# Optimization experiments

Measured on AMD Instinct MI355X. Metric: run time of the kernel, lower is better.

## Reference

```python
import jax, jax.numpy as jnp
import numpy as np

NUM_ITER = 10
NUM_LAYER = 3
EMB_DIM = 128
ALPHA = 0.1
NUM_ATOM_FEATS = 9
ATOM_VOCAB = 119
N_NODES = 50000
N_EDGES = 800000


def setup_inputs() -> dict:
    key = jax.random.key(0)
    ks = jax.random.split(key, 5)
    x = jax.random.randint(ks[0], (N_NODES, NUM_ATOM_FEATS), 0, ATOM_VOCAB, dtype=jnp.int64 if jax.config.jax_enable_x64 else jnp.int32)
    edge_index = jax.random.randint(ks[1], (2, N_EDGES), 0, N_NODES, dtype=jnp.int32)
    scale = 1.0 / np.sqrt(EMB_DIM)
    atom_emb = jax.random.normal(ks[2], (NUM_ATOM_FEATS, ATOM_VOCAB, EMB_DIM), dtype=jnp.float32) * 0.1
    Ws = jax.random.normal(ks[3], (NUM_LAYER, EMB_DIM, EMB_DIM), dtype=jnp.float32) * scale
    bs = jax.random.normal(ks[4], (NUM_LAYER, EMB_DIM), dtype=jnp.float32) * 0.01
    return {"x": x, "edge_index": edge_index, "atom_emb": atom_emb, "Ws": Ws, "bs": bs}


def _forward(x, edge_index, atom_emb, Ws, bs):
    N = x.shape[0]
    # AtomEncoder: sum of per-feature-column embeddings -> [N, d]
    h = jax.vmap(lambda tbl, ids: tbl[ids], in_axes=(0, 1))(atom_emb, x).sum(axis=0)
    # MLP stack with ReLU on all but last layer
    L = Ws.shape[0]
    for l in range(L):
        h = h @ Ws[l] + bs[l]
        if l != L - 1:
            h = jax.nn.relu(h)
    # gcn_norm with self loops, unit edge weights (eval mode: no edge dropout)
    self_idx = jnp.arange(N, dtype=edge_index.dtype)
    src = jnp.concatenate([edge_index[0], self_idx])
    dst = jnp.concatenate([edge_index[1], self_idx])
    deg = jax.ops.segment_sum(jnp.ones(src.shape[0], dtype=h.dtype), dst, num_segments=N)
    dinv = jnp.where(deg > 0, jax.lax.rsqrt(jnp.maximum(deg, 1e-12)), 0.0)
    coef = (dinv[src] * dinv[dst])[:, None]  # [E+N, 1]
    h0 = h
    def body(i, h):
        agg = jax.ops.segment_sum(coef * h[src], dst, num_segments=N)
        return (1.0 - ALPHA) * agg + ALPHA * h0
    h = jax.lax.fori_loop(0, NUM_ITER, body, h)
    return h  # JK == 'last'


def reference(x, edge_index, atom_emb, Ws, bs):
    return _forward(x, edge_index, atom_emb, Ws, bs)
```

## Files before the change

### kernel.cpp

```cpp
#include <hip/hip_runtime.h>

#define N_NODES 50000
#define N_EDGES 800000
#define EMB 128
#define NFEAT 9
#define VOCAB 119
#define NITER 10
#define ALPHA 0.1f


__device__ inline unsigned int f2bf1(float x) {
    union { float f; unsigned u; } v; v.f = x;
    unsigned r = v.u + 0x7fffu + ((v.u >> 16) & 1u);
    return r >> 16;
}
__device__ inline unsigned int f2bf2(float lo, float hi) {
    return f2bf1(lo) | (f2bf1(hi) << 16);
}
__device__ inline float bf2f_lo(unsigned u) {
    union { unsigned u; float f; } v; v.u = u << 16; return v.f;
}
__device__ inline float bf2f_hi(unsigned u) {
    union { unsigned u; float f; } v; v.u = u & 0xffff0000u; return v.f;
}


__global__ void k_zero(int* __restrict__ cnt, int* __restrict__ cursor) {
    int i = blockIdx.x * blockDim.x + threadIdx.x;
    if (i < N_NODES) { cnt[i] = 0; cursor[i] = 0; }
}

__global__ void k_count(const int* __restrict__ dst, int* __restrict__ cnt) {
    int e = blockIdx.x * blockDim.x + threadIdx.x;
    if (e < N_EDGES) atomicAdd(&cnt[dst[e]], 1);
}

__global__ void k_dinv(const int* __restrict__ cnt, float* __restrict__ dinv) {
    int v = blockIdx.x * blockDim.x + threadIdx.x;
    if (v < N_NODES) dinv[v] = rsqrtf((float)(cnt[v] + 1));
}

__global__ void k_scan1(const int* __restrict__ cnt, int* __restrict__ rowptr,
                        int* __restrict__ bsum) {
    __shared__ int s[256];
    int t = threadIdx.x;
    int idx = blockIdx.x * 256 + t;
    int v = (idx < N_NODES) ? cnt[idx] : 0;
    s[t] = v; __syncthreads();
    for (int off = 1; off < 256; off <<= 1) {
        int add = (t >= off) ? s[t - off] : 0;
        __syncthreads();
        s[t] += add;
        __syncthreads();
    }
    if (idx < N_NODES) rowptr[idx] = s[t] - v;
    if (t == 255) bsum[blockIdx.x] = s[255];
}

__global__ void k_scan2(int* __restrict__ bsum, int nb) {
    __shared__ int s[256];
    int t = threadIdx.x;
    int v = (t < nb) ? bsum[t] : 0;
    s[t] = v; __syncthreads();
    for (int off = 1; off < 256; off <<= 1) {
        int add = (t >= off) ? s[t - off] : 0;
        __syncthreads();
        s[t] += add;
        __syncthreads();
    }
    if (t < nb) bsum[t] = s[t] - v;
}

__global__ void k_scan3(int* __restrict__ rowptr, const int* __restrict__ bsum) {
    int idx = blockIdx.x * 256 + threadIdx.x;
    if (idx < N_NODES) rowptr[idx] += bsum[blockIdx.x];
}

__global__ void k_fill(const int* __restrict__ src, const int* __restrict__ dst,
                       const int* __restrict__ rowptr, int* __restrict__ cursor,
                       int* __restrict__ csr_src) {
    int e = blockIdx.x * blockDim.x + threadIdx.x;
    if (e < N_EDGES) {
        int v = dst[e];
        int pos = rowptr[v] + atomicAdd(&cursor[v], 1);
        csr_src[pos] = src[e];
    }
}


__global__ void k_encode(const int* __restrict__ x, const float* __restrict__ emb,
                         float* __restrict__ out) {
    int t = threadIdx.x;
    int d = t & 127, sub = t >> 7;
    int n = blockIdx.x * 2 + sub;
    if (n >= N_NODES) return;
    const int* xr = x + n * NFEAT;
    float s = 0.f;
#pragma unroll
    for (int f = 0; f < NFEAT; ++f) {
        int id = xr[f];
        s += emb[(f * VOCAB + id) * EMB + d];
    }
    out[n * EMB + d] = s;
}


__device__ inline void fma4(float4& acc, float4 a, float4 w0, float4 w1,
                            float4 w2, float4 w3) {
    acc.x = fmaf(a.x, w0.x, fmaf(a.y, w1.x, fmaf(a.z, w2.x, fmaf(a.w, w3.x, acc.x))));
    acc.y = fmaf(a.x, w0.y, fmaf(a.y, w1.y, fmaf(a.z, w2.y, fmaf(a.w, w3.y, acc.y))));
    acc.z = fmaf(a.x, w0.z, fmaf(a.y, w1.z, fmaf(a.z, w2.z, fmaf(a.w, w3.z, acc.z))));
    acc.w = fmaf(a.x, w0.w, fmaf(a.y, w1.w, fmaf(a.z, w2.w, fmaf(a.w, w3.w, acc.w))));
}

__device__ inline float4 relu4(float4 a) {
    return make_float4(fmaxf(a.x, 0.f), fmaxf(a.y, 0.f), fmaxf(a.z, 0.f), fmaxf(a.w, 0.f));
}

template <int RELU, int WQ>
__global__ __launch_bounds__(256) void k_mlp(const float* __restrict__ in,
                                             float* __restrict__ out,
                                             const float* __restrict__ W,
                                             const float* __restrict__ b,
                                             const float* __restrict__ dinv,
                                             uint2* __restrict__ q0out) {
    __shared__ float4 Wl[EMB * 32];
    __shared__ float4 hs[32 * 32];
    int t = threadIdx.x;
    const float4* W4 = (const float4*)W;
    for (int i = t; i < EMB * 32; i += 256) Wl[i] = W4[i];
    int base = blockIdx.x * 32;
    const float4* in4 = (const float4*)in;
    for (int i = t; i < 32 * 32; i += 256) {
        int n = base + (i >> 5);
        hs[i] = (n < N_NODES) ? in4[n * 32 + (i & 31)] : make_float4(0.f, 0.f, 0.f, 0.f);
    }
    __syncthreads();
    int q = t & 31;
    int g = t >> 5;
    float4 bias = ((const float4*)b)[q];
    float4 acc0 = bias, acc1 = bias, acc2 = bias, acc3 = bias;
    const float4* h0r = &hs[(g * 4 + 0) * 32];
    const float4* h1r = &hs[(g * 4 + 1) * 32];
    const float4* h2r = &hs[(g * 4 + 2) * 32];
    const float4* h3r = &hs[(g * 4 + 3) * 32];
#pragma unroll 2
    for (int k0 = 0; k0 < EMB; k0 += 4) {
        float4 w0 = Wl[(k0 + 0) * 32 + q];
        float4 w1 = Wl[(k0 + 1) * 32 + q];
        float4 w2 = Wl[(k0 + 2) * 32 + q];
        float4 w3 = Wl[(k0 + 3) * 32 + q];
        int kq = k0 >> 2;
        fma4(acc0, h0r[kq], w0, w1, w2, w3);
        fma4(acc1, h1r[kq], w0, w1, w2, w3);
        fma4(acc2, h2r[kq], w0, w1, w2, w3);
        fma4(acc3, h3r[kq], w0, w1, w2, w3);
    }
    if (RELU) {
        acc0 = relu4(acc0); acc1 = relu4(acc1);
        acc2 = relu4(acc2); acc3 = relu4(acc3);
    }
    float4* out4 = (float4*)out;
    int n0 = base + g * 4;
    if (n0 + 0 < N_NODES) out4[(n0 + 0) * 32 + q] = acc0;
    if (n0 + 1 < N_NODES) out4[(n0 + 1) * 32 + q] = acc1;
    if (n0 + 2 < N_NODES) out4[(n0 + 2) * 32 + q] = acc2;
    if (n0 + 3 < N_NODES) out4[(n0 + 3) * 32 + q] = acc3;
    if (WQ) {
        if (n0 + 0 < N_NODES) {
            float s = dinv[n0 + 0];
            q0out[(n0 + 0) * 32 + q] =
                make_uint2(f2bf2(acc0.x * s, acc0.y * s), f2bf2(acc0.z * s, acc0.w * s));
        }
        if (n0 + 1 < N_NODES) {
            float s = dinv[n0 + 1];
            q0out[(n0 + 1) * 32 + q] =
                make_uint2(f2bf2(acc1.x * s, acc1.y * s), f2bf2(acc1.z * s, acc1.w * s));
        }
        if (n0 + 2 < N_NODES) {
            float s = dinv[n0 + 2];
            q0out[(n0 + 2) * 32 + q] =
                make_uint2(f2bf2(acc2.x * s, acc2.y * s), f2bf2(acc2.z * s, acc2.w * s));
        }
        if (n0 + 3 < N_NODES) {
            float s = dinv[n0 + 3];
            q0out[(n0 + 3) * 32 + q] =
                make_uint2(f2bf2(acc3.x * s, acc3.y * s), f2bf2(acc3.z * s, acc3.w * s));
        }
    }
}


#define ACC8(g) \
    a0 += bf2f_lo((g).x); a1 += bf2f_hi((g).x); \
    a2 += bf2f_lo((g).y); a3 += bf2f_hi((g).y); \
    a4 += bf2f_lo((g).z); a5 += bf2f_hi((g).z); \
    a6 += bf2f_lo((g).w); a7 += bf2f_hi((g).w);

template <int LAST>
__global__ __launch_bounds__(256) void k_prop(const uint4* __restrict__ qin,
                                              const float4* __restrict__ h0,
                                              void* __restrict__ outb,
                                              const int* __restrict__ rowptr,
                                              const int* __restrict__ cnt,
                                              const int* __restrict__ csr_src,
                                              const float* __restrict__ dinv) {
    int t = threadIdx.x;
    int lane = t & 63;
    int pair = lane >> 4;
    int dq = lane & 15;
    int v = blockIdx.x * 4 + (t >> 6);
    int start = rowptr[v];
    int c = cnt[v];
    const int* cs = csr_src + start;
    float a0 = 0.f, a1 = 0.f, a2 = 0.f, a3 = 0.f;
    float a4 = 0.f, a5 = 0.f, a6 = 0.f, a7 = 0.f;
    int i = 0;
    for (; i + 8 <= c; i += 8) {
        int s0 = cs[i + pair];
        int s1 = cs[i + 4 + pair];
        uint4 g0 = qin[s0 * 16 + dq];
        uint4 g1 = qin[s1 * 16 + dq];
        ACC8(g0);
        ACC8(g1);
    }
    for (; i < c; i += 4) {
        int e = i + pair;
        if (e < c) {
            uint4 g = qin[cs[e] * 16 + dq];
            ACC8(g);
        }
    }
    a0 += __shfl_xor(a0, 16); a0 += __shfl_xor(a0, 32);
    a1 += __shfl_xor(a1, 16); a1 += __shfl_xor(a1, 32);
    a2 += __shfl_xor(a2, 16); a2 += __shfl_xor(a2, 32);
    a3 += __shfl_xor(a3, 16); a3 += __shfl_xor(a3, 32);
    a4 += __shfl_xor(a4, 16); a4 += __shfl_xor(a4, 32);
    a5 += __shfl_xor(a5, 16); a5 += __shfl_xor(a5, 32);
    a6 += __shfl_xor(a6, 16); a6 += __shfl_xor(a6, 32);
    a7 += __shfl_xor(a7, 16); a7 += __shfl_xor(a7, 32);

    float dv = dinv[v];
    uint4 qv = qin[v * 16 + dq];
    float4 hlo = h0[v * 32 + 2 * dq];
    float4 hhi = h0[v * 32 + 2 * dq + 1];
    float h_0 = (1.f - ALPHA) * dv * (a0 + bf2f_lo(qv.x)) + ALPHA * hlo.x;
    float h_1 = (1.f - ALPHA) * dv * (a1 + bf2f_hi(qv.x)) + ALPHA * hlo.y;
    float h_2 = (1.f - ALPHA) * dv * (a2 + bf2f_lo(qv.y)) + ALPHA * hlo.z;
    float h_3 = (1.f - ALPHA) * dv * (a3 + bf2f_hi(qv.y)) + ALPHA * hlo.w;
    float h_4 = (1.f - ALPHA) * dv * (a4 + bf2f_lo(qv.z)) + ALPHA * hhi.x;
    float h_5 = (1.f - ALPHA) * dv * (a5 + bf2f_hi(qv.z)) + ALPHA * hhi.y;
    float h_6 = (1.f - ALPHA) * dv * (a6 + bf2f_lo(qv.w)) + ALPHA * hhi.z;
    float h_7 = (1.f - ALPHA) * dv * (a7 + bf2f_hi(qv.w)) + ALPHA * hhi.w;

    if (LAST) {
        if (pair < 2) {
            float4 wv = (pair == 0) ? make_float4(h_0, h_1, h_2, h_3)
                                    : make_float4(h_4, h_5, h_6, h_7);
            ((float4*)outb)[v * 32 + 2 * dq + pair] = wv;
        }
    } else {
        if (pair == 0) {
            uint4 wv;
            wv.x = f2bf2(h_0 * dv, h_1 * dv);
            wv.y = f2bf2(h_2 * dv, h_3 * dv);
            wv.z = f2bf2(h_4 * dv, h_5 * dv);
            wv.w = f2bf2(h_6 * dv, h_7 * dv);
            ((uint4*)outb)[v * 16 + dq] = wv;
        }
    }
}


extern "C" void kernel_launch(void* const* d_in, const int* in_sizes, int n_in,
                              void* d_out, int out_size, void* d_ws, size_t ws_size,
                              hipStream_t stream) {
    const int*   x    = (const int*)d_in[0];
    const int*   ei   = (const int*)d_in[1];
    const float* emb  = (const float*)d_in[2];
    const float* Ws   = (const float*)d_in[3];
    const float* bs   = (const float*)d_in[4];
    float* out = (float*)d_out;

    const int* src = ei;
    const int* dst = ei + N_EDGES;

    char* w = (char*)d_ws;
    size_t off = 0;
    auto alloc = [&](size_t bytes) {
        void* p = w + off;
        off += (bytes + 255) & ~(size_t)255;
        return p;
    };
    float* h0      = (float*)alloc((size_t)N_NODES * EMB * 4);
    float* hT      = (float*)alloc((size_t)N_NODES * EMB * 4);
    float* hU      = (float*)alloc((size_t)N_NODES * EMB * 4);
    void*  qA      = alloc((size_t)N_NODES * EMB * 2);
    void*  qB      = alloc((size_t)N_NODES * EMB * 2);
    float* dinv    = (float*)alloc(N_NODES * 4);
    int*   cnt     = (int*)alloc(N_NODES * 4);
    int*   cursor  = (int*)alloc(N_NODES * 4);
    int*   rowptr  = (int*)alloc(N_NODES * 4);
    int*   bsum    = (int*)alloc(256 * 4);
    int*   csr_src = (int*)alloc(N_EDGES * 4);
    (void)ws_size; (void)n_in; (void)in_sizes; (void)out_size;

    const int NB_N  = (N_NODES + 255) / 256;
    const int NB_E  = (N_EDGES + 255) / 256;
    const int NB_2N = (N_NODES + 1) / 2;
    const int NB_M  = (N_NODES + 31) / 32;
    const int NB_P  = N_NODES / 4;

    k_zero<<<NB_N, 256, 0, stream>>>(cnt, cursor);
    k_count<<<NB_E, 256, 0, stream>>>(dst, cnt);
    k_dinv<<<NB_N, 256, 0, stream>>>(cnt, dinv);
    k_scan1<<<NB_N, 256, 0, stream>>>(cnt, rowptr, bsum);
    k_scan2<<<1, 256, 0, stream>>>(bsum, NB_N);
    k_scan3<<<NB_N, 256, 0, stream>>>(rowptr, bsum);
    k_fill<<<NB_E, 256, 0, stream>>>(src, dst, rowptr, cursor, csr_src);

    k_encode<<<NB_2N, 256, 0, stream>>>(x, emb, hT);
    k_mlp<1, 0><<<NB_M, 256, 0, stream>>>(hT, hU, Ws + 0 * EMB * EMB, bs + 0 * EMB,
                                          nullptr, nullptr);
    k_mlp<1, 0><<<NB_M, 256, 0, stream>>>(hU, hT, Ws + 1 * EMB * EMB, bs + 1 * EMB,
                                          nullptr, nullptr);
    k_mlp<0, 1><<<NB_M, 256, 0, stream>>>(hT, h0, Ws + 2 * EMB * EMB, bs + 2 * EMB,
                                          dinv, (uint2*)qA);

    const uint4* qin = (const uint4*)qA;
    for (int i = 0; i < NITER; ++i) {
        if (i == NITER - 1) {
            k_prop<1><<<NB_P, 256, 0, stream>>>(qin, (const float4*)h0, out,
                                                rowptr, cnt, csr_src, dinv);
        } else {
            void* qo = (i & 1) ? qA : qB;
            k_prop<0><<<NB_P, 256, 0, stream>>>(qin, (const float4*)h0, qo,
                                                rowptr, cnt, csr_src, dinv);
            qin = (const uint4*)qo;
        }
    }
}
```

Measured before the change: 643.7 us.

## Store bf16 h0 for propagation, widen edge-index loads, and streamline CSR build

Intermediate propagation steps now read a bf16 copy of h0 written by the last MLP layer, which halves that per-iteration read, while the final step still uses the fp32 h0. The gather loop loads source indices as 16-byte vectors, unrolls to 16 edges per step, and moves the row pointer and count into scalar registers with readfirstlane. CSR construction keeps the per-edge atomic slot from the counting pass so the fill needs no second atomic, and the dinv kernel is folded into the scan. The MLP runs in place, dropping one buffer. The bf16 h0 adds rounding error in intermediate steps, and the in-place MLP relies on each block loading its input tile into shared memory before writing.

```diff
diff --git a/kernel.cpp b/kernel.cpp
--- a/kernel.cpp
+++ b/kernel.cpp
@@ -24,28 +24,27 @@
     union { unsigned u; float f; } v; v.u = u & 0xffff0000u; return v.f;
 }
 
-
-__global__ void k_zero(int* __restrict__ cnt, int* __restrict__ cursor) {
+struct __attribute__((aligned(4))) i4 { int x, y, z, w; };
+
+
+__global__ void k_zero(int* __restrict__ cnt) {
     int i = blockIdx.x * blockDim.x + threadIdx.x;
-    if (i < N_NODES) { cnt[i] = 0; cursor[i] = 0; }
-}
-
-__global__ void k_count(const int* __restrict__ dst, int* __restrict__ cnt) {
+    if (i < N_NODES) cnt[i] = 0;
+}
+
+__global__ void k_count(const int* __restrict__ dst, int* __restrict__ cnt,
+                        int* __restrict__ ord) {
     int e = blockIdx.x * blockDim.x + threadIdx.x;
-    if (e < N_EDGES) atomicAdd(&cnt[dst[e]], 1);
-}
-
-__global__ void k_dinv(const int* __restrict__ cnt, float* __restrict__ dinv) {
-    int v = blockIdx.x * blockDim.x + threadIdx.x;
-    if (v < N_NODES) dinv[v] = rsqrtf((float)(cnt[v] + 1));
+    if (e < N_EDGES) ord[e] = atomicAdd(&cnt[dst[e]], 1);
 }
 
 __global__ void k_scan1(const int* __restrict__ cnt, int* __restrict__ rowptr,
-                        int* __restrict__ bsum) {
+                        int* __restrict__ bsum, float* __restrict__ dinv) {
     __shared__ int s[256];
     int t = threadIdx.x;
     int idx = blockIdx.x * 256 + t;
     int v = (idx < N_NODES) ? cnt[idx] : 0;
+    if (idx < N_NODES) dinv[idx] = rsqrtf((float)(v + 1));
     s[t] = v; __syncthreads();
     for (int off = 1; off < 256; off <<= 1) {
         int add = (t >= off) ? s[t - off] : 0;
@@ -77,13 +76,11 @@
 }
 
 __global__ void k_fill(const int* __restrict__ src, const int* __restrict__ dst,
-                       const int* __restrict__ rowptr, int* __restrict__ cursor,
+                       const int* __restrict__ ord, const int* __restrict__ rowptr,
                        int* __restrict__ csr_src) {
     int e = blockIdx.x * blockDim.x + threadIdx.x;
     if (e < N_EDGES) {
-        int v = dst[e];
-        int pos = rowptr[v] + atomicAdd(&cursor[v], 1);
-        csr_src[pos] = src[e];
+        csr_src[rowptr[dst[e]] + ord[e]] = src[e];
     }
 }
 
@@ -123,7 +120,8 @@
                                              const float* __restrict__ W,
                                              const float* __restrict__ b,
                                              const float* __restrict__ dinv,
-                                             uint2* __restrict__ q0out) {
+                                             uint2* __restrict__ q0out,
+                                             uint2* __restrict__ h0bout) {
     __shared__ float4 Wl[EMB * 32];
     __shared__ float4 hs[32 * 32];
     int t = threadIdx.x;
@@ -167,25 +165,17 @@
     if (n0 + 2 < N_NODES) out4[(n0 + 2) * 32 + q] = acc2;
     if (n0 + 3 < N_NODES) out4[(n0 + 3) * 32 + q] = acc3;
     if (WQ) {
-        if (n0 + 0 < N_NODES) {
-            float s = dinv[n0 + 0];
-            q0out[(n0 + 0) * 32 + q] =
-                make_uint2(f2bf2(acc0.x * s, acc0.y * s), f2bf2(acc0.z * s, acc0.w * s));
-        }
-        if (n0 + 1 < N_NODES) {
-            float s = dinv[n0 + 1];
-            q0out[(n0 + 1) * 32 + q] =
-                make_uint2(f2bf2(acc1.x * s, acc1.y * s), f2bf2(acc1.z * s, acc1.w * s));
-        }
-        if (n0 + 2 < N_NODES) {
-            float s = dinv[n0 + 2];
-            q0out[(n0 + 2) * 32 + q] =
-                make_uint2(f2bf2(acc2.x * s, acc2.y * s), f2bf2(acc2.z * s, acc2.w * s));
-        }
-        if (n0 + 3 < N_NODES) {
-            float s = dinv[n0 + 3];
-            q0out[(n0 + 3) * 32 + q] =
-                make_uint2(f2bf2(acc3.x * s, acc3.y * s), f2bf2(acc3.z * s, acc3.w * s));
+#pragma unroll
+        for (int j = 0; j < 4; ++j) {
+            int n = n0 + j;
+            if (n < N_NODES) {
+                float4 a = (j == 0) ? acc0 : (j == 1) ? acc1 : (j == 2) ? acc2 : acc3;
+                float s = dinv[n];
+                q0out[n * 32 + q] =
+                    make_uint2(f2bf2(a.x * s, a.y * s), f2bf2(a.z * s, a.w * s));
+                h0bout[n * 32 + q] =
+                    make_uint2(f2bf2(a.x, a.y), f2bf2(a.z, a.w));
+            }
         }
     }
 }
@@ -197,9 +187,12 @@
     a4 += bf2f_lo((g).z); a5 += bf2f_hi((g).z); \
     a6 += bf2f_lo((g).w); a7 += bf2f_hi((g).w);
 
+#define SEL(iv) (pair == 0 ? (iv).x : pair == 1 ? (iv).y : pair == 2 ? (iv).z : (iv).w)
+
 template <int LAST>
 __global__ __launch_bounds__(256) void k_prop(const uint4* __restrict__ qin,
                                               const float4* __restrict__ h0,
+                                              const uint4* __restrict__ h0b,
                                               void* __restrict__ outb,
                                               const int* __restrict__ rowptr,
                                               const int* __restrict__ cnt,
@@ -210,19 +203,31 @@
     int pair = lane >> 4;
     int dq = lane & 15;
     int v = blockIdx.x * 4 + (t >> 6);
-    int start = rowptr[v];
-    int c = cnt[v];
+    int start = __builtin_amdgcn_readfirstlane(rowptr[v]);
+    int c = __builtin_amdgcn_readfirstlane(cnt[v]);
     const int* cs = csr_src + start;
     float a0 = 0.f, a1 = 0.f, a2 = 0.f, a3 = 0.f;
     float a4 = 0.f, a5 = 0.f, a6 = 0.f, a7 = 0.f;
     int i = 0;
-    for (; i + 8 <= c; i += 8) {
-        int s0 = cs[i + pair];
-        int s1 = cs[i + 4 + pair];
+    for (; i + 16 <= c; i += 16) {
+        i4 ia = *(const i4*)(cs + i);
+        i4 ib = *(const i4*)(cs + i + 4);
+        i4 ic = *(const i4*)(cs + i + 8);
+        i4 id = *(const i4*)(cs + i + 12);
+        int s0 = SEL(ia), s1 = SEL(ib), s2 = SEL(ic), s3 = SEL(id);
         uint4 g0 = qin[s0 * 16 + dq];
         uint4 g1 = qin[s1 * 16 + dq];
-        ACC8(g0);
-        ACC8(g1);
+        uint4 g2 = qin[s2 * 16 + dq];
+        uint4 g3 = qin[s3 * 16 + dq];
+        ACC8(g0); ACC8(g1); ACC8(g2); ACC8(g3);
+    }
+    for (; i + 8 <= c; i += 8) {
+        i4 ia = *(const i4*)(cs + i);
+        i4 ib = *(const i4*)(cs + i + 4);
+        int s0 = SEL(ia), s1 = SEL(ib);
+        uint4 g0 = qin[s0 * 16 + dq];
+        uint4 g1 = qin[s1 * 16 + dq];
+        ACC8(g0); ACC8(g1);
     }
     for (; i < c; i += 4) {
         int e = i + pair;
@@ -242,24 +247,38 @@
 
     float dv = dinv[v];
     uint4 qv = qin[v * 16 + dq];
-    float4 hlo = h0[v * 32 + 2 * dq];
-    float4 hhi = h0[v * 32 + 2 * dq + 1];
-    float h_0 = (1.f - ALPHA) * dv * (a0 + bf2f_lo(qv.x)) + ALPHA * hlo.x;
-    float h_1 = (1.f - ALPHA) * dv * (a1 + bf2f_hi(qv.x)) + ALPHA * hlo.y;
-    float h_2 = (1.f - ALPHA) * dv * (a2 + bf2f_lo(qv.y)) + ALPHA * hlo.z;
-    float h_3 = (1.f - ALPHA) * dv * (a3 + bf2f_hi(qv.y)) + ALPHA * hlo.w;
-    float h_4 = (1.f - ALPHA) * dv * (a4 + bf2f_lo(qv.z)) + ALPHA * hhi.x;
-    float h_5 = (1.f - ALPHA) * dv * (a5 + bf2f_hi(qv.z)) + ALPHA * hhi.y;
-    float h_6 = (1.f - ALPHA) * dv * (a6 + bf2f_lo(qv.w)) + ALPHA * hhi.z;
-    float h_7 = (1.f - ALPHA) * dv * (a7 + bf2f_hi(qv.w)) + ALPHA * hhi.w;
+    float s0 = a0 + bf2f_lo(qv.x), s1 = a1 + bf2f_hi(qv.x);
+    float s2 = a2 + bf2f_lo(qv.y), s3 = a3 + bf2f_hi(qv.y);
+    float s4 = a4 + bf2f_lo(qv.z), s5 = a5 + bf2f_hi(qv.z);
+    float s6 = a6 + bf2f_lo(qv.w), s7 = a7 + bf2f_hi(qv.w);
+    const float K = 1.f - ALPHA;
 
     if (LAST) {
+        float4 hlo = h0[v * 32 + 2 * dq];
+        float4 hhi = h0[v * 32 + 2 * dq + 1];
+        float h_0 = K * dv * s0 + ALPHA * hlo.x;
+        float h_1 = K * dv * s1 + ALPHA * hlo.y;
+        float h_2 = K * dv * s2 + ALPHA * hlo.z;
+        float h_3 = K * dv * s3 + ALPHA * hlo.w;
+        float h_4 = K * dv * s4 + ALPHA * hhi.x;
+        float h_5 = K * dv * s5 + ALPHA * hhi.y;
+        float h_6 = K * dv * s6 + ALPHA * hhi.z;
+        float h_7 = K * dv * s7 + ALPHA * hhi.w;
         if (pair < 2) {
             float4 wv = (pair == 0) ? make_float4(h_0, h_1, h_2, h_3)
                                     : make_float4(h_4, h_5, h_6, h_7);
             ((float4*)outb)[v * 32 + 2 * dq + pair] = wv;
         }
     } else {
+        uint4 hv = h0b[v * 16 + dq];
+        float h_0 = K * dv * s0 + ALPHA * bf2f_lo(hv.x);
+        float h_1 = K * dv * s1 + ALPHA * bf2f_hi(hv.x);
+        float h_2 = K * dv * s2 + ALPHA * bf2f_lo(hv.y);
+        float h_3 = K * dv * s3 + ALPHA * bf2f_hi(hv.y);
+        float h_4 = K * dv * s4 + ALPHA * bf2f_lo(hv.z);
+        float h_5 = K * dv * s5 + ALPHA * bf2f_hi(hv.z);
+        float h_6 = K * dv * s6 + ALPHA * bf2f_lo(hv.w);
+        float h_7 = K * dv * s7 + ALPHA * bf2f_hi(hv.w);
         if (pair == 0) {
             uint4 wv;
             wv.x = f2bf2(h_0 * dv, h_1 * dv);
@@ -294,15 +313,15 @@
     };
     float* h0      = (float*)alloc((size_t)N_NODES * EMB * 4);
     float* hT      = (float*)alloc((size_t)N_NODES * EMB * 4);
-    float* hU      = (float*)alloc((size_t)N_NODES * EMB * 4);
     void*  qA      = alloc((size_t)N_NODES * EMB * 2);
     void*  qB      = alloc((size_t)N_NODES * EMB * 2);
+    void*  h0b     = alloc((size_t)N_NODES * EMB * 2);
     float* dinv    = (float*)alloc(N_NODES * 4);
     int*   cnt     = (int*)alloc(N_NODES * 4);
-    int*   cursor  = (int*)alloc(N_NODES * 4);
     int*   rowptr  = (int*)alloc(N_NODES * 4);
     int*   bsum    = (int*)alloc(256 * 4);
     int*   csr_src = (int*)alloc(N_EDGES * 4);
+    int*   ord     = (int*)alloc(N_EDGES * 4);
     (void)ws_size; (void)n_in; (void)in_sizes; (void)out_size;
 
     const int NB_N  = (N_NODES + 255) / 256;
@@ -311,30 +330,31 @@
     const int NB_M  = (N_NODES + 31) / 32;
     const int NB_P  = N_NODES / 4;
 
-    k_zero<<<NB_N, 256, 0, stream>>>(cnt, cursor);
-    k_count<<<NB_E, 256, 0, stream>>>(dst, cnt);
-    k_dinv<<<NB_N, 256, 0, stream>>>(cnt, dinv);
-    k_scan1<<<NB_N, 256, 0, stream>>>(cnt, rowptr, bsum);
+    k_zero<<<NB_N, 256, 0, stream>>>(cnt);
+    k_count<<<NB_E, 256, 0, stream>>>(dst, cnt, ord);
+    k_scan1<<<NB_N, 256, 0, stream>>>(cnt, rowptr, bsum, dinv);
     k_scan2<<<1, 256, 0, stream>>>(bsum, NB_N);
     k_scan3<<<NB_N, 256, 0, stream>>>(rowptr, bsum);
-    k_fill<<<NB_E, 256, 0, stream>>>(src, dst, rowptr, cursor, csr_src);
+    k_fill<<<NB_E, 256, 0, stream>>>(src, dst, ord, rowptr, csr_src);
 
     k_encode<<<NB_2N, 256, 0, stream>>>(x, emb, hT);
-    k_mlp<1, 0><<<NB_M, 256, 0, stream>>>(hT, hU, Ws + 0 * EMB * EMB, bs + 0 * EMB,
-                                          nullptr, nullptr);
-    k_mlp<1, 0><<<NB_M, 256, 0, stream>>>(hU, hT, Ws + 1 * EMB * EMB, bs + 1 * EMB,
-                                          nullptr, nullptr);
+    k_mlp<1, 0><<<NB_M, 256, 0, stream>>>(hT, hT, Ws + 0 * EMB * EMB, bs + 0 * EMB,
+                                          nullptr, nullptr, nullptr);
+    k_mlp<1, 0><<<NB_M, 256, 0, stream>>>(hT, hT, Ws + 1 * EMB * EMB, bs + 1 * EMB,
+                                          nullptr, nullptr, nullptr);
     k_mlp<0, 1><<<NB_M, 256, 0, stream>>>(hT, h0, Ws + 2 * EMB * EMB, bs + 2 * EMB,
-                                          dinv, (uint2*)qA);
+                                          dinv, (uint2*)qA, (uint2*)h0b);
 
     const uint4* qin = (const uint4*)qA;
     for (int i = 0; i < NITER; ++i) {
         if (i == NITER - 1) {
-            k_prop<1><<<NB_P, 256, 0, stream>>>(qin, (const float4*)h0, out,
+            k_prop<1><<<NB_P, 256, 0, stream>>>(qin, (const float4*)h0,
+                                                (const uint4*)h0b, out,
                                                 rowptr, cnt, csr_src, dinv);
         } else {
             void* qo = (i & 1) ? qA : qB;
-            k_prop<0><<<NB_P, 256, 0, stream>>>(qin, (const float4*)h0, qo,
+            k_prop<0><<<NB_P, 256, 0, stream>>>(qin, (const float4*)h0,
+                                                (const uint4*)h0b, qo,
                                                 rowptr, cnt, csr_src, dinv);
             qin = (const uint4*)qo;
         }
```

Measured after the change: 589.7 us. -8.4%, faster.
